# Performance work log

Measured on AMD Instinct MI355X. Metric: run time of the kernel, lower is better.

## Reference

```python
import jax, jax.numpy as jnp
import numpy as np

B, N, M, D = 2, 256, 8, 256      # batch, seq, modalities, dmodel
H, DH = 8, 64                     # heads, dim_head (hardcoded defaults)
INNER = H * DH                    # 512
MULT = 4                          # FFN mult
SCALE = DH ** -0.5
EPS = 1e-5


def layer_norm(x, g, b):
    mu = jnp.mean(x, axis=-1, keepdims=True)
    var = jnp.mean((x - mu) ** 2, axis=-1, keepdims=True)
    return (x - mu) * jax.lax.rsqrt(var + EPS) * g + b


def setup_inputs() -> dict:
    key = jax.random.key(0)
    ks = jax.random.split(key, 8)
    s = 0.02
    return {
        "x": jax.random.normal(ks[0], (B, D, M, N), jnp.float32),
        "Wq": jax.random.normal(ks[1], (D, INNER), jnp.float32) * s,
        "Wkv": jax.random.normal(ks[2], (D, 2 * INNER), jnp.float32) * s,
        "Wout": jax.random.normal(ks[3], (INNER * M, D * M), jnp.float32) * s,
        "bout": jnp.zeros((D * M,), jnp.float32),
        "g1": jnp.ones((D,), jnp.float32),
        "beta1": jnp.zeros((D,), jnp.float32),
        "Wff1": jax.random.normal(ks[4], (D, 2 * D * MULT), jnp.float32) * s,
        "bff1": jnp.zeros((2 * D * MULT,), jnp.float32),
        "Wff2": jax.random.normal(ks[5], (D * MULT, D), jnp.float32) * s,
        "bff2": jnp.zeros((D,), jnp.float32),
        "g2": jnp.ones((D,), jnp.float32),
        "beta2": jnp.zeros((D,), jnp.float32),
    }


def reference(x, Wq, Wkv, Wout, bout, g1, beta1, Wff1, bff1, Wff2, bff2, g2, beta2):
    x_shape = x.shape
    xt = jnp.transpose(x, (0, 3, 2, 1))          # [B,N,M,D]
    # --- Channel_Seq_Big_Attention (self-attention, context = x) ---
    q = (xt @ Wq).reshape(B, N, M, H, DH)
    kv = xt @ Wkv
    k, v = jnp.split(kv, 2, axis=-1)
    k = k.reshape(B, N, M, H, DH)
    v = v.reshape(B, N, M, H, DH)
    # sim: [(b h), i, j, m, z] kept as [B,H,i,j,m,z]
    sim = jnp.einsum('bimhd,bjzhd->bhijmz', q, k) * SCALE
    attn = jax.nn.softmax(sim, axis=2)           # softmax over j (dim=-3 of bijmz)
    out = jnp.einsum('bhijmz,bjmhd->bizhd', attn, v)  # [B,N,M,H,DH]
    out = out.reshape(B, N, M * H * DH)          # 'b n (m h d)'
    o = (out @ Wout + bout).reshape(B, N, M, D)
    # --- residual + post-norm ---
    xt = layer_norm(xt + o, g1, beta1)
    # --- GEGLU FFN ---
    hg = xt @ Wff1 + bff1
    a, gate = jnp.split(hg, 2, axis=-1)
    ff = (a * jax.nn.gelu(gate, approximate=False)) @ Wff2 + bff2
    xt = layer_norm(xt + ff, g2, beta2)
    return xt.reshape(x_shape)                   # torch .view(x_shape)
```

## Files before the change

kernel.cpp:

```cpp
#include <hip/hip_runtime.h>
#include <math.h>

#define KS_ 0.1803368801111244f

typedef __attribute__((ext_vector_type(8))) short bf16x8;
typedef __attribute__((ext_vector_type(4))) short bf16x4;
typedef __attribute__((ext_vector_type(4))) float f32x4;

__device__ inline short f2bf(float f) {
  unsigned u = __builtin_bit_cast(unsigned, f);
  u += 0x7fff + ((u >> 16) & 1);
  return (short)(u >> 16);
}

__global__ __launch_bounds__(256) void k_transpose(const float* __restrict__ x, float* __restrict__ xt,
                                                   short* __restrict__ xtbf) {
  __shared__ float tile[32][33];
  int bm = blockIdx.z; int b = bm >> 3; int m = bm & 7;
  int d0 = blockIdx.x * 32, n0 = blockIdx.y * 32;
#pragma unroll
  for (int r = 0; r < 32; r += 8) {
    int d = d0 + threadIdx.y + r, n = n0 + threadIdx.x;
    tile[threadIdx.y + r][threadIdx.x] = x[((size_t)(b * 256 + d) * 8 + m) * 256 + n];
  }
  __syncthreads();
#pragma unroll
  for (int r = 0; r < 32; r += 8) {
    int n = n0 + threadIdx.y + r, d = d0 + threadIdx.x;
    float v = tile[threadIdx.x][threadIdx.y + r];
    size_t idx = ((size_t)(b * 256 + n) * 8 + m) * 256 + d;
    xt[idx] = v;
    xtbf[idx] = f2bf(v);
  }
}

__global__ __launch_bounds__(256) void k_wt(const float* __restrict__ W, short* __restrict__ WT, int K, int N) {
  __shared__ float tile[32][33];
  int n0 = blockIdx.x * 32, k0 = blockIdx.y * 32;
  int tx = threadIdx.x & 31, ty = threadIdx.x >> 5;
#pragma unroll
  for (int r = 0; r < 32; r += 8)
    tile[ty + r][tx] = W[(size_t)(k0 + ty + r) * N + n0 + tx];
  __syncthreads();
#pragma unroll
  for (int r = 0; r < 32; r += 8)
    WT[(size_t)(n0 + ty + r) * K + k0 + tx] = f2bf(tile[tx][ty + r]);
}

__global__ __launch_bounds__(256) void k_gemm_bf(const short* __restrict__ A, const short* __restrict__ Bt,
                                                 const float* __restrict__ bias, float* __restrict__ C,
                                                 int M, int N, int K, int Ks) {
  __shared__ short As[64 * 40];
  __shared__ short Bs[64 * 40];
  int t = threadIdx.x;
  int row0 = blockIdx.y * 64, col0 = blockIdx.x * 64;
  int kp = blockIdx.z;
  int kbeg = kp * Ks, kend = kbeg + Ks;
  int w = t >> 6, lane = t & 63, quad = lane >> 4, l16 = lane & 15;
  int wr = w >> 1, wc = w & 1;
  int lrow = t >> 2, lch = (t & 3) * 8;
  const short* Ap = A + (size_t)(row0 + lrow) * K + lch;
  const short* Bp = Bt + (size_t)(col0 + lrow) * K + lch;
  f32x4 acc[2][2] = {{{0,0,0,0},{0,0,0,0}},{{0,0,0,0},{0,0,0,0}}};
  bf16x8 av = *(const bf16x8*)(Ap + kbeg);
  bf16x8 bv = *(const bf16x8*)(Bp + kbeg);
  for (int k0 = kbeg; k0 < kend; k0 += 32) {
    *(bf16x8*)&As[lrow * 40 + lch] = av;
    *(bf16x8*)&Bs[lrow * 40 + lch] = bv;
    __syncthreads();
    if (k0 + 32 < kend) {
      av = *(const bf16x8*)(Ap + k0 + 32);
      bv = *(const bf16x8*)(Bp + k0 + 32);
    }
    bf16x8 af[2], bf[2];
#pragma unroll
    for (int rf = 0; rf < 2; rf++) af[rf] = *(const bf16x8*)&As[(wr * 32 + rf * 16 + l16) * 40 + quad * 8];
#pragma unroll
    for (int cf = 0; cf < 2; cf++) bf[cf] = *(const bf16x8*)&Bs[(wc * 32 + cf * 16 + l16) * 40 + quad * 8];
#pragma unroll
    for (int rf = 0; rf < 2; rf++)
#pragma unroll
      for (int cf = 0; cf < 2; cf++)
        acc[rf][cf] = __builtin_amdgcn_mfma_f32_16x16x32_bf16(af[rf], bf[cf], acc[rf][cf], 0, 0, 0);
    __syncthreads();
  }
  float* Cp = C + (size_t)kp * M * N;
#pragma unroll
  for (int rf = 0; rf < 2; rf++)
#pragma unroll
    for (int cf = 0; cf < 2; cf++) {
      int col = col0 + wc * 32 + cf * 16 + l16;
      float vb = (bias && kp == 0) ? bias[col] : 0.0f;
#pragma unroll
      for (int r = 0; r < 4; r++) {
        int row = row0 + wr * 32 + rf * 16 + quad * 4 + r;
        Cp[(size_t)row * N + col] = acc[rf][cf][r] + vb;
      }
    }
}

__global__ __launch_bounds__(256) void k_ff1g(const short* __restrict__ A, const short* __restrict__ Bt,
                                              const float* __restrict__ bias, short* __restrict__ gg) {
  __shared__ short As[64 * 40];
  __shared__ short Ba[64 * 40];
  __shared__ short Bg[64 * 40];
  int t = threadIdx.x;
  int colA0 = blockIdx.x * 64, row0 = blockIdx.y * 64;
  int w = t >> 6, lane = t & 63, quad = lane >> 4, l16 = lane & 15;
  int wr = w >> 1, wc = w & 1;
  int lrow = t >> 2, lch = (t & 3) * 8;
  const short* Ap  = A + (size_t)(row0 + lrow) * 256 + lch;
  const short* Bpa = Bt + (size_t)(colA0 + lrow) * 256 + lch;
  const short* Bpg = Bt + (size_t)(1024 + colA0 + lrow) * 256 + lch;
  f32x4 za = {0, 0, 0, 0};
  f32x4 acc_a[2][2] = {{za, za}, {za, za}};
  f32x4 acc_g[2][2] = {{za, za}, {za, za}};
  bf16x8 av = *(const bf16x8*)(Ap);
  bf16x8 bva = *(const bf16x8*)(Bpa);
  bf16x8 bvg = *(const bf16x8*)(Bpg);
  for (int k0 = 0; k0 < 256; k0 += 32) {
    *(bf16x8*)&As[lrow * 40 + lch] = av;
    *(bf16x8*)&Ba[lrow * 40 + lch] = bva;
    *(bf16x8*)&Bg[lrow * 40 + lch] = bvg;
    __syncthreads();
    if (k0 + 32 < 256) {
      av  = *(const bf16x8*)(Ap + k0 + 32);
      bva = *(const bf16x8*)(Bpa + k0 + 32);
      bvg = *(const bf16x8*)(Bpg + k0 + 32);
    }
    bf16x8 af[2], ba[2], bg[2];
#pragma unroll
    for (int rf = 0; rf < 2; rf++) af[rf] = *(const bf16x8*)&As[(wr * 32 + rf * 16 + l16) * 40 + quad * 8];
#pragma unroll
    for (int cf = 0; cf < 2; cf++) {
      ba[cf] = *(const bf16x8*)&Ba[(wc * 32 + cf * 16 + l16) * 40 + quad * 8];
      bg[cf] = *(const bf16x8*)&Bg[(wc * 32 + cf * 16 + l16) * 40 + quad * 8];
    }
#pragma unroll
    for (int rf = 0; rf < 2; rf++)
#pragma unroll
      for (int cf = 0; cf < 2; cf++) {
        acc_a[rf][cf] = __builtin_amdgcn_mfma_f32_16x16x32_bf16(af[rf], ba[cf], acc_a[rf][cf], 0, 0, 0);
        acc_g[rf][cf] = __builtin_amdgcn_mfma_f32_16x16x32_bf16(af[rf], bg[cf], acc_g[rf][cf], 0, 0, 0);
      }
    __syncthreads();
  }
#pragma unroll
  for (int rf = 0; rf < 2; rf++)
#pragma unroll
    for (int cf = 0; cf < 2; cf++) {
      int col = colA0 + wc * 32 + cf * 16 + l16;
      float ba_ = bias[col], bg_ = bias[1024 + col];
#pragma unroll
      for (int r = 0; r < 4; r++) {
        int row = row0 + wr * 32 + rf * 16 + quad * 4 + r;
        float a = acc_a[rf][cf][r] + ba_;
        float g = acc_g[rf][cf][r] + bg_;
        float ge = 0.5f * g * (1.0f + erff(g * 0.70710678118654752f));
        gg[(size_t)row * 1024 + col] = f2bf(a * ge);
      }
    }
}

__global__ __launch_bounds__(256) void k_prep_qfrag(const float* __restrict__ qkv, short* __restrict__ qfrag) {
  int c = blockIdx.x * 256 + threadIdx.x;
  int lane = c & 63, ks = (c >> 6) & 1, rt = (c >> 7) & 127, bh = c >> 14;
  int b = bh >> 3, h = bh & 7;
  int m = rt >> 4, i = ((rt & 15) << 4) + (lane & 15);
  int d = ks * 32 + (lane >> 4) * 8;
  const float* src = qkv + (size_t)((b * 256 + i) * 8 + m) * 1536 + h * 64 + d;
  float4 f0 = *(const float4*)src, f1 = *(const float4*)(src + 4);
  bf16x8 o;
  o[0] = f2bf(f0.x); o[1] = f2bf(f0.y); o[2] = f2bf(f0.z); o[3] = f2bf(f0.w);
  o[4] = f2bf(f1.x); o[5] = f2bf(f1.y); o[6] = f2bf(f1.z); o[7] = f2bf(f1.w);
  *(bf16x8*)(qfrag + (size_t)c * 8) = o;
}

__global__ __launch_bounds__(256) void k_prep_kfrag(const float* __restrict__ qkv, short* __restrict__ kfrag) {
  int c = blockIdx.x * 256 + threadIdx.x;
  int lane = c & 63, ks = (c >> 6) & 1, rt = (c >> 7) & 127, bh = c >> 14;
  int b = bh >> 3, h = bh & 7;
  int z = rt >> 4, j = ((rt & 15) << 4) + (lane & 15);
  int d = ks * 32 + (lane >> 4) * 8;
  const float* src = qkv + (size_t)((b * 256 + j) * 8 + z) * 1536 + 512 + h * 64 + d;
  float4 f0 = *(const float4*)src, f1 = *(const float4*)(src + 4);
  bf16x8 o;
  o[0] = f2bf(f0.x); o[1] = f2bf(f0.y); o[2] = f2bf(f0.z); o[3] = f2bf(f0.w);
  o[4] = f2bf(f1.x); o[5] = f2bf(f1.y); o[6] = f2bf(f1.z); o[7] = f2bf(f1.w);
  *(bf16x8*)(kfrag + (size_t)c * 8) = o;
}

__global__ __launch_bounds__(256) void k_prep_vfrag(const float* __restrict__ qkv, short* __restrict__ vfrag) {
  __shared__ float Vs[256 * 66];
  int jc = blockIdx.x, bh = blockIdx.y;
  int b = bh >> 3, h = bh & 7;
  int t = threadIdx.x;
#pragma unroll
  for (int cc = 0; cc < 16; cc++) {
    int c = cc * 256 + t;
    int row = c >> 4, ch = c & 15;
    int m = row >> 5, jl = row & 31;
    float4 f = *(const float4*)(qkv + (size_t)((b * 256 + jc * 32 + jl) * 8 + m) * 1536 + 1024 + h * 64 + ch * 4);
    *(float4*)&Vs[row * 66 + ch * 4] = f;
  }
  __syncthreads();
  int m0 = t >> 6, lane = t & 63, quad = lane >> 4, l16 = lane & 15;
#pragma unroll
  for (int dt = 0; dt < 4; dt++)
#pragma unroll
    for (int jf = 0; jf < 2; jf++) {
      bf16x8 o;
#pragma unroll
      for (int e = 0; e < 8; e++) {
        int row = (2 * m0 + (e >> 2)) * 32 + jf * 16 + quad * 4 + (e & 3);
        o[e] = f2bf(Vs[row * 66 + dt * 16 + l16]);
      }
      size_t cid = ((((size_t)(bh * 8 + jc) * 4 + m0) * 4 + dt) * 2 + jf) * 64 + lane;
      *(bf16x8*)(vfrag + cid * 8) = o;
    }
}

__global__ __launch_bounds__(256) void k_attn_den5(const short* __restrict__ qfrag, const short* __restrict__ kfrag,
                                                   float* __restrict__ rdg) {
  int ct2 = blockIdx.x, mp = blockIdx.y, bh = blockIdx.z;
  int t = threadIdx.x;
  int w = t >> 6, lane = t & 63;
  int rt0 = ct2 * 8 + w * 2;
  bf16x8 bfr[2][2];
#pragma unroll
  for (int cf = 0; cf < 2; cf++)
#pragma unroll
    for (int ks = 0; ks < 2; ks++)
      bfr[cf][ks] = *(const bf16x8*)(kfrag + ((size_t)((bh * 128 + rt0 + cf) * 2 + ks)) * 512 + lane * 8);
  for (int mi = 0; mi < 2; mi++) {
    int m = mp * 2 + mi;
    float fa0 = 0.0f, fa1 = 0.0f;
#pragma unroll 4
    for (int it2 = 0; it2 < 16; it2++) {
      const short* ap = qfrag + ((size_t)((bh * 128 + m * 16 + it2) * 2)) * 512 + lane * 8;
      bf16x8 a0 = *(const bf16x8*)ap;
      bf16x8 a1 = *(const bf16x8*)(ap + 512);
      f32x4 c0 = {0, 0, 0, 0}, c1 = {0, 0, 0, 0};
      c0 = __builtin_amdgcn_mfma_f32_16x16x32_bf16(a0, bfr[0][0], c0, 0, 0, 0);
      c0 = __builtin_amdgcn_mfma_f32_16x16x32_bf16(a1, bfr[0][1], c0, 0, 0, 0);
      c1 = __builtin_amdgcn_mfma_f32_16x16x32_bf16(a0, bfr[1][0], c1, 0, 0, 0);
      c1 = __builtin_amdgcn_mfma_f32_16x16x32_bf16(a1, bfr[1][1], c1, 0, 0, 0);
#pragma unroll
      for (int r = 0; r < 4; r++) {
        fa0 += __builtin_amdgcn_exp2f(c0[r] * KS_);
        fa1 += __builtin_amdgcn_exp2f(c1[r] * KS_);
      }
    }
    fa0 += __shfl_xor(fa0, 16); fa0 += __shfl_xor(fa0, 32);
    fa1 += __shfl_xor(fa1, 16); fa1 += __shfl_xor(fa1, 32);
    if (lane < 16) {
      rdg[(size_t)(bh * 8 + m) * 2048 + rt0 * 16 + lane] = -__builtin_amdgcn_logf(fa0);
      rdg[(size_t)(bh * 8 + m) * 2048 + (rt0 + 1) * 16 + lane] = -__builtin_amdgcn_logf(fa1);
    }
  }
}

__global__ __launch_bounds__(256) void k_attn_out5(const short* __restrict__ qfrag, const short* __restrict__ kfrag,
                                                   const short* __restrict__ vfrag, const float* __restrict__ rdg,
                                                   short* __restrict__ ao) {
  __shared__ float red[4 * 64 * 17];
  int z = blockIdx.x, itp = blockIdx.y, bh = blockIdx.z;
  int b = bh >> 3, h = bh & 7;
  int t = threadIdx.x, w = t >> 6, lane = t & 63, quad = lane >> 4, l16 = lane & 15;
  const float* rb = rdg + (size_t)bh * 16384;
  f32x4 z4 = {0, 0, 0, 0};
  bf16x8 qf[2][2][2];
#pragma unroll
  for (int iti = 0; iti < 2; iti++)
#pragma unroll
    for (int mm = 0; mm < 2; mm++)
#pragma unroll
      for (int ks = 0; ks < 2; ks++)
        qf[iti][mm][ks] = *(const bf16x8*)(qfrag +
            ((size_t)((bh * 128 + (2 * w + mm) * 16 + itp * 2 + iti) * 2 + ks)) * 512 + lane * 8);
  f32x4 acc[2][4];
#pragma unroll
  for (int iti = 0; iti < 2; iti++)
#pragma unroll
    for (int dt = 0; dt < 4; dt++) acc[iti][dt] = z4;
  for (int jc = 0; jc < 8; jc++) {
    bf16x8 vf[4][2];
#pragma unroll
    for (int dt = 0; dt < 4; dt++)
#pragma unroll
      for (int jf = 0; jf < 2; jf++)
        vf[dt][jf] = *(const bf16x8*)(vfrag + ((((size_t)(bh * 8 + jc) * 4 + w) * 4 + dt) * 2 + jf) * 512 + lane * 8);
    bf16x8 kf[2][2];
#pragma unroll
    for (int jf = 0; jf < 2; jf++) {
      const short* kp = kfrag + ((size_t)((bh * 128 + z * 16 + jc * 2 + jf) * 2)) * 512 + lane * 8;
      kf[jf][0] = *(const bf16x8*)kp;
      kf[jf][1] = *(const bf16x8*)(kp + 512);
    }
    float n0[2][4], n1[2][4];
#pragma unroll
    for (int jf = 0; jf < 2; jf++) {
      float4 nv0 = *(const float4*)(rb + (size_t)(2 * w) * 2048 + z * 256 + jc * 32 + jf * 16 + quad * 4);
      float4 nv1 = *(const float4*)(rb + (size_t)(2 * w + 1) * 2048 + z * 256 + jc * 32 + jf * 16 + quad * 4);
      n0[jf][0] = nv0.x; n0[jf][1] = nv0.y; n0[jf][2] = nv0.z; n0[jf][3] = nv0.w;
      n1[jf][0] = nv1.x; n1[jf][1] = nv1.y; n1[jf][2] = nv1.z; n1[jf][3] = nv1.w;
    }
#pragma unroll
    for (int iti = 0; iti < 2; iti++) {
      f32x4 c[2][2] = {{z4, z4}, {z4, z4}};
#pragma unroll
      for (int jf = 0; jf < 2; jf++)
#pragma unroll
        for (int mm = 0; mm < 2; mm++) {
          c[jf][mm] = __builtin_amdgcn_mfma_f32_16x16x32_bf16(kf[jf][0], qf[iti][mm][0], c[jf][mm], 0, 0, 0);
          c[jf][mm] = __builtin_amdgcn_mfma_f32_16x16x32_bf16(kf[jf][1], qf[iti][mm][1], c[jf][mm], 0, 0, 0);
        }
      bf16x8 pf[2];
#pragma unroll
      for (int jf = 0; jf < 2; jf++) {
        unsigned u[8];
#pragma unroll
        for (int e = 0; e < 4; e++) {
          u[e]     = __builtin_bit_cast(unsigned, __builtin_amdgcn_exp2f(fmaf(c[jf][0][e], KS_, n0[jf][e]))) + 0x8000u;
          u[e + 4] = __builtin_bit_cast(unsigned, __builtin_amdgcn_exp2f(fmaf(c[jf][1][e], KS_, n1[jf][e]))) + 0x8000u;
        }
        uint4 pv;
        pv.x = __builtin_amdgcn_perm(u[1], u[0], 0x07060302u);
        pv.y = __builtin_amdgcn_perm(u[3], u[2], 0x07060302u);
        pv.z = __builtin_amdgcn_perm(u[5], u[4], 0x07060302u);
        pv.w = __builtin_amdgcn_perm(u[7], u[6], 0x07060302u);
        pf[jf] = __builtin_bit_cast(bf16x8, pv);
      }
#pragma unroll
      for (int dt = 0; dt < 4; dt++)
#pragma unroll
        for (int jf = 0; jf < 2; jf++)
          acc[iti][dt] = __builtin_amdgcn_mfma_f32_16x16x32_bf16(vf[dt][jf], pf[jf], acc[iti][dt], 0, 0, 0);
    }
  }
  for (int iti = 0; iti < 2; iti++) {
#pragma unroll
    for (int dt = 0; dt < 4; dt++)
#pragma unroll
      for (int r = 0; r < 4; r++)
        red[w * 1088 + (dt * 16 + quad * 4 + r) * 17 + l16] = acc[iti][dt][r];
    __syncthreads();
    {
      int i = t >> 4, dg = t & 15;
      float s[4] = {0, 0, 0, 0};
#pragma unroll
      for (int w2 = 0; w2 < 4; w2++)
#pragma unroll
        for (int r2 = 0; r2 < 4; r2++)
          s[r2] += red[w2 * 1088 + (dg * 4 + r2) * 17 + i];
      bf16x4 ov;
#pragma unroll
      for (int r2 = 0; r2 < 4; r2++) ov[r2] = f2bf(s[r2]);
      *(bf16x4*)(ao + (size_t)((b * 256 + itp * 32 + iti * 16 + i) * 8 + z) * 512 + h * 64 + dg * 4) = ov;
    }
    __syncthreads();
  }
}

__global__ __launch_bounds__(256) void k_ln(const float* __restrict__ X, const float* __restrict__ P, int np,
                                            const float* __restrict__ g, const float* __restrict__ be,
                                            float* __restrict__ Y, short* __restrict__ Ybf) {
  __shared__ float sm[8];
  int row = blockIdx.x, t = threadIdx.x;
  int lane = t & 63, w = t >> 6;
  size_t base = (size_t)row * 256;
  float v = X[base + t];
  for (int p = 0; p < np; p++) v += P[(size_t)p * 1048576 + base + t];
  float s = v;
  s += __shfl_xor(s, 1); s += __shfl_xor(s, 2); s += __shfl_xor(s, 4);
  s += __shfl_xor(s, 8); s += __shfl_xor(s, 16); s += __shfl_xor(s, 32);
  if (lane == 0) sm[w] = s;
  __syncthreads();
  float mu = (sm[0] + sm[1] + sm[2] + sm[3]) * (1.0f / 256.0f);
  float dv = v - mu;
  float s2 = dv * dv;
  s2 += __shfl_xor(s2, 1); s2 += __shfl_xor(s2, 2); s2 += __shfl_xor(s2, 4);
  s2 += __shfl_xor(s2, 8); s2 += __shfl_xor(s2, 16); s2 += __shfl_xor(s2, 32);
  if (lane == 0) sm[4 + w] = s2;
  __syncthreads();
  float var = (sm[4] + sm[5] + sm[6] + sm[7]) * (1.0f / 256.0f);
  float rs = rsqrtf(var + 1e-5f);
  float res = dv * rs * g[t] + be[t];
  Y[base + t] = res;
  if (Ybf) Ybf[base + t] = f2bf(res);
}

extern "C" void kernel_launch(void* const* d_in, const int* in_sizes, int n_in,
                              void* d_out, int out_size, void* d_ws, size_t ws_size,
                              hipStream_t stream) {
  const float* x    = (const float*)d_in[0];
  const float* Wq   = (const float*)d_in[1];
  const float* Wkv  = (const float*)d_in[2];
  const float* Wout = (const float*)d_in[3];
  const float* bout = (const float*)d_in[4];
  const float* g1   = (const float*)d_in[5];
  const float* be1  = (const float*)d_in[6];
  const float* Wff1 = (const float*)d_in[7];
  const float* bff1 = (const float*)d_in[8];
  const float* Wff2 = (const float*)d_in[9];
  const float* bff2 = (const float*)d_in[10];
  const float* g2   = (const float*)d_in[11];
  const float* be2  = (const float*)d_in[12];
  float* out = (float*)d_out;
  float* w = (float*)d_ws;

  float* xt   = w;
  float* qkv  = w + 1048576;
  float* part = w + 1048576;
  float* y    = w + 9437184;
  float* rdg  = w + 11534336;
  short* sb     = (short*)(w + 11796480);
  short* qfrag  = sb;
  short* kfrag  = sb + 2097152;
  short* vfrag  = sb + 4194304;
  short* xt_bf  = sb + 6291456;
  short* ao_bf  = sb + 7340032;
  short* y_bf   = sb + 9437184;
  short* gg_bf  = sb + 10485760;
  short* WqkvT  = sb + 14680064;
  short* WoutT  = sb + 15073280;
  short* Wff1T  = sb + 23461888;
  short* Wff2T  = sb + 23986176;

  k_transpose<<<dim3(8, 8, 16), dim3(32, 8), 0, stream>>>(x, xt, xt_bf);
  k_wt<<<dim3(16, 8), 256, 0, stream>>>(Wq, WqkvT, 256, 512);
  k_wt<<<dim3(32, 8), 256, 0, stream>>>(Wkv, WqkvT + 131072, 256, 1024);
  k_wt<<<dim3(64, 128), 256, 0, stream>>>(Wout, WoutT, 4096, 2048);
  k_wt<<<dim3(64, 8), 256, 0, stream>>>(Wff1, Wff1T, 256, 2048);
  k_wt<<<dim3(8, 32), 256, 0, stream>>>(Wff2, Wff2T, 1024, 256);
  k_gemm_bf<<<dim3(24, 64, 1), 256, 0, stream>>>(xt_bf, WqkvT, nullptr, qkv, 4096, 1536, 256, 256);
  k_prep_qfrag<<<1024, 256, 0, stream>>>(qkv, qfrag);
  k_prep_kfrag<<<1024, 256, 0, stream>>>(qkv, kfrag);
  k_prep_vfrag<<<dim3(8, 16), 256, 0, stream>>>(qkv, vfrag);
  k_attn_den5<<<dim3(16, 4, 16), 256, 0, stream>>>(qfrag, kfrag, rdg);
  k_attn_out5<<<dim3(8, 8, 16), 256, 0, stream>>>(qfrag, kfrag, vfrag, rdg, ao_bf);
  k_gemm_bf<<<dim3(32, 8, 4), 256, 0, stream>>>(ao_bf, WoutT, bout, part, 512, 2048, 4096, 1024);
  k_ln<<<4096, 256, 0, stream>>>(xt, part, 4, g1, be1, y, y_bf);
  k_ff1g<<<dim3(16, 64), 256, 0, stream>>>(y_bf, Wff1T, bff1, gg_bf);
  k_gemm_bf<<<dim3(4, 64, 4), 256, 0, stream>>>(gg_bf, Wff2T, bff2, part, 4096, 256, 1024, 256);
  k_ln<<<4096, 256, 0, stream>>>(y, part, 4, g2, be2, out, nullptr);
}
```

Measured before the change: 239.3 us.

## Merge prep kernels into single launches and prefetch next K/V chunk in attention

Six transpose/weight-conversion launches are folded into one block-indexed k_prep_all kernel, and the Q and K fragment prep kernels become one launch selected by block index. This cuts launch count and the idle gaps between small kernels. In the attention output kernel, V/K fragments and normalizer values for the next j-chunk are loaded before the current chunk's MFMAs run, so global load latency overlaps compute. The cost is higher register pressure in that kernel, which may lower occupancy.

```diff
diff --git a/kernel.cpp b/kernel.cpp
--- a/kernel.cpp
+++ b/kernel.cpp
@@ -13,31 +13,10 @@
   return (short)(u >> 16);
 }
 
-__global__ __launch_bounds__(256) void k_transpose(const float* __restrict__ x, float* __restrict__ xt,
-                                                   short* __restrict__ xtbf) {
-  __shared__ float tile[32][33];
-  int bm = blockIdx.z; int b = bm >> 3; int m = bm & 7;
-  int d0 = blockIdx.x * 32, n0 = blockIdx.y * 32;
-#pragma unroll
-  for (int r = 0; r < 32; r += 8) {
-    int d = d0 + threadIdx.y + r, n = n0 + threadIdx.x;
-    tile[threadIdx.y + r][threadIdx.x] = x[((size_t)(b * 256 + d) * 8 + m) * 256 + n];
-  }
-  __syncthreads();
-#pragma unroll
-  for (int r = 0; r < 32; r += 8) {
-    int n = n0 + threadIdx.y + r, d = d0 + threadIdx.x;
-    float v = tile[threadIdx.x][threadIdx.y + r];
-    size_t idx = ((size_t)(b * 256 + n) * 8 + m) * 256 + d;
-    xt[idx] = v;
-    xtbf[idx] = f2bf(v);
-  }
-}
-
-__global__ __launch_bounds__(256) void k_wt(const float* __restrict__ W, short* __restrict__ WT, int K, int N) {
-  __shared__ float tile[32][33];
-  int n0 = blockIdx.x * 32, k0 = blockIdx.y * 32;
-  int tx = threadIdx.x & 31, ty = threadIdx.x >> 5;
+__device__ inline void wt_tile(const float* __restrict__ W, short* __restrict__ WT,
+                               int K, int N, int bx, int by, int t, float (*tile)[33]) {
+  int n0 = bx * 32, k0 = by * 32;
+  int tx = t & 31, ty = t >> 5;
 #pragma unroll
   for (int r = 0; r < 32; r += 8)
     tile[ty + r][tx] = W[(size_t)(k0 + ty + r) * N + n0 + tx];
@@ -45,6 +24,52 @@
 #pragma unroll
   for (int r = 0; r < 32; r += 8)
     WT[(size_t)(n0 + ty + r) * K + k0 + tx] = f2bf(tile[tx][ty + r]);
+}
+
+__global__ __launch_bounds__(256) void k_prep_all(const float* __restrict__ x, float* __restrict__ xt,
+                                                  short* __restrict__ xtbf,
+                                                  const float* __restrict__ Wq, const float* __restrict__ Wkv,
+                                                  const float* __restrict__ Wout, const float* __restrict__ Wff1,
+                                                  const float* __restrict__ Wff2,
+                                                  short* __restrict__ WqkvT, short* __restrict__ WoutT,
+                                                  short* __restrict__ Wff1T, short* __restrict__ Wff2T) {
+  __shared__ float tile[32][33];
+  int bid = blockIdx.x, t = threadIdx.x;
+  if (bid < 8192) {
+    wt_tile(Wout, WoutT, 4096, 2048, bid & 63, bid >> 6, t, tile);
+  } else if (bid < 9216) {
+    int r = bid - 8192;
+    int bx = r & 7, by = (r >> 3) & 7, bm = r >> 6;
+    int b = bm >> 3, m = bm & 7;
+    int d0 = bx * 32, n0 = by * 32;
+    int tx = t & 31, ty = t >> 5;
+#pragma unroll
+    for (int rr = 0; rr < 32; rr += 8) {
+      int d = d0 + ty + rr, n = n0 + tx;
+      tile[ty + rr][tx] = x[((size_t)(b * 256 + d) * 8 + m) * 256 + n];
+    }
+    __syncthreads();
+#pragma unroll
+    for (int rr = 0; rr < 32; rr += 8) {
+      int n = n0 + ty + rr, d = d0 + tx;
+      float v = tile[tx][ty + rr];
+      size_t idx = ((size_t)(b * 256 + n) * 8 + m) * 256 + d;
+      xt[idx] = v;
+      xtbf[idx] = f2bf(v);
+    }
+  } else if (bid < 9344) {
+    int r = bid - 9216;
+    wt_tile(Wq, WqkvT, 256, 512, r & 15, r >> 4, t, tile);
+  } else if (bid < 9600) {
+    int r = bid - 9344;
+    wt_tile(Wkv, WqkvT + 131072, 256, 1024, r & 31, r >> 5, t, tile);
+  } else if (bid < 10112) {
+    int r = bid - 9600;
+    wt_tile(Wff1, Wff1T, 256, 2048, r & 63, r >> 6, t, tile);
+  } else {
+    int r = bid - 10112;
+    wt_tile(Wff2, Wff2T, 1024, 256, r & 7, r >> 3, t, tile);
+  }
 }
 
 __global__ __launch_bounds__(256) void k_gemm_bf(const short* __restrict__ A, const short* __restrict__ Bt,
@@ -162,32 +187,22 @@
     }
 }
 
-__global__ __launch_bounds__(256) void k_prep_qfrag(const float* __restrict__ qkv, short* __restrict__ qfrag) {
-  int c = blockIdx.x * 256 + threadIdx.x;
+__global__ __launch_bounds__(256) void k_prep_qk(const float* __restrict__ qkv, short* __restrict__ qfrag,
+                                                 short* __restrict__ kfrag) {
+  int bid = blockIdx.x;
+  int sel = bid >> 10;
+  int c = (bid & 1023) * 256 + threadIdx.x;
   int lane = c & 63, ks = (c >> 6) & 1, rt = (c >> 7) & 127, bh = c >> 14;
   int b = bh >> 3, h = bh & 7;
-  int m = rt >> 4, i = ((rt & 15) << 4) + (lane & 15);
+  int mz = rt >> 4, ij = ((rt & 15) << 4) + (lane & 15);
   int d = ks * 32 + (lane >> 4) * 8;
-  const float* src = qkv + (size_t)((b * 256 + i) * 8 + m) * 1536 + h * 64 + d;
+  const float* src = qkv + (size_t)((b * 256 + ij) * 8 + mz) * 1536 + sel * 512 + h * 64 + d;
   float4 f0 = *(const float4*)src, f1 = *(const float4*)(src + 4);
   bf16x8 o;
   o[0] = f2bf(f0.x); o[1] = f2bf(f0.y); o[2] = f2bf(f0.z); o[3] = f2bf(f0.w);
   o[4] = f2bf(f1.x); o[5] = f2bf(f1.y); o[6] = f2bf(f1.z); o[7] = f2bf(f1.w);
-  *(bf16x8*)(qfrag + (size_t)c * 8) = o;
-}
-
-__global__ __launch_bounds__(256) void k_prep_kfrag(const float* __restrict__ qkv, short* __restrict__ kfrag) {
-  int c = blockIdx.x * 256 + threadIdx.x;
-  int lane = c & 63, ks = (c >> 6) & 1, rt = (c >> 7) & 127, bh = c >> 14;
-  int b = bh >> 3, h = bh & 7;
-  int z = rt >> 4, j = ((rt & 15) << 4) + (lane & 15);
-  int d = ks * 32 + (lane >> 4) * 8;
-  const float* src = qkv + (size_t)((b * 256 + j) * 8 + z) * 1536 + 512 + h * 64 + d;
-  float4 f0 = *(const float4*)src, f1 = *(const float4*)(src + 4);
-  bf16x8 o;
-  o[0] = f2bf(f0.x); o[1] = f2bf(f0.y); o[2] = f2bf(f0.z); o[3] = f2bf(f0.w);
-  o[4] = f2bf(f1.x); o[5] = f2bf(f1.y); o[6] = f2bf(f1.z); o[7] = f2bf(f1.w);
-  *(bf16x8*)(kfrag + (size_t)c * 8) = o;
+  short* dst = sel ? kfrag : qfrag;
+  *(bf16x8*)(dst + (size_t)c * 8) = o;
 }
 
 __global__ __launch_bounds__(256) void k_prep_vfrag(const float* __restrict__ qkv, short* __restrict__ vfrag) {
@@ -260,7 +275,7 @@
   }
 }
 
-__global__ __launch_bounds__(256) void k_attn_out5(const short* __restrict__ qfrag, const short* __restrict__ kfrag,
+__global__ __launch_bounds__(256) void k_attn_out6(const short* __restrict__ qfrag, const short* __restrict__ kfrag,
                                                    const short* __restrict__ vfrag, const float* __restrict__ rdg,
                                                    short* __restrict__ ao) {
   __shared__ float red[4 * 64 * 17];
@@ -283,28 +298,42 @@
   for (int iti = 0; iti < 2; iti++)
 #pragma unroll
     for (int dt = 0; dt < 4; dt++) acc[iti][dt] = z4;
+  bf16x8 vf[4][2], kf[2][2];
+  float4 nv0[2], nv1[2];
+#pragma unroll
+  for (int dt = 0; dt < 4; dt++)
+#pragma unroll
+    for (int jf = 0; jf < 2; jf++)
+      vf[dt][jf] = *(const bf16x8*)(vfrag + ((((size_t)(bh * 8 + 0) * 4 + w) * 4 + dt) * 2 + jf) * 512 + lane * 8);
+#pragma unroll
+  for (int jf = 0; jf < 2; jf++) {
+    const short* kp = kfrag + ((size_t)((bh * 128 + z * 16 + 0 * 2 + jf) * 2)) * 512 + lane * 8;
+    kf[jf][0] = *(const bf16x8*)kp;
+    kf[jf][1] = *(const bf16x8*)(kp + 512);
+    nv0[jf] = *(const float4*)(rb + (size_t)(2 * w) * 2048 + z * 256 + 0 * 32 + jf * 16 + quad * 4);
+    nv1[jf] = *(const float4*)(rb + (size_t)(2 * w + 1) * 2048 + z * 256 + 0 * 32 + jf * 16 + quad * 4);
+  }
   for (int jc = 0; jc < 8; jc++) {
-    bf16x8 vf[4][2];
-#pragma unroll
-    for (int dt = 0; dt < 4; dt++)
-#pragma unroll
-      for (int jf = 0; jf < 2; jf++)
-        vf[dt][jf] = *(const bf16x8*)(vfrag + ((((size_t)(bh * 8 + jc) * 4 + w) * 4 + dt) * 2 + jf) * 512 + lane * 8);
-    bf16x8 kf[2][2];
-#pragma unroll
-    for (int jf = 0; jf < 2; jf++) {
-      const short* kp = kfrag + ((size_t)((bh * 128 + z * 16 + jc * 2 + jf) * 2)) * 512 + lane * 8;
-      kf[jf][0] = *(const bf16x8*)kp;
-      kf[jf][1] = *(const bf16x8*)(kp + 512);
-    }
-    float n0[2][4], n1[2][4];
-#pragma unroll
-    for (int jf = 0; jf < 2; jf++) {
-      float4 nv0 = *(const float4*)(rb + (size_t)(2 * w) * 2048 + z * 256 + jc * 32 + jf * 16 + quad * 4);
-      float4 nv1 = *(const float4*)(rb + (size_t)(2 * w + 1) * 2048 + z * 256 + jc * 32 + jf * 16 + quad * 4);
-      n0[jf][0] = nv0.x; n0[jf][1] = nv0.y; n0[jf][2] = nv0.z; n0[jf][3] = nv0.w;
-      n1[jf][0] = nv1.x; n1[jf][1] = nv1.y; n1[jf][2] = nv1.z; n1[jf][3] = nv1.w;
-    }
+    bf16x8 vfn[4][2], kfn[2][2];
+    float4 nv0n[2], nv1n[2];
+    if (jc < 7) {
+      int jn = jc + 1;
+#pragma unroll
+      for (int dt = 0; dt < 4; dt++)
+#pragma unroll
+        for (int jf = 0; jf < 2; jf++)
+          vfn[dt][jf] = *(const bf16x8*)(vfrag + ((((size_t)(bh * 8 + jn) * 4 + w) * 4 + dt) * 2 + jf) * 512 + lane * 8);
+#pragma unroll
+      for (int jf = 0; jf < 2; jf++) {
+        const short* kp = kfrag + ((size_t)((bh * 128 + z * 16 + jn * 2 + jf) * 2)) * 512 + lane * 8;
+        kfn[jf][0] = *(const bf16x8*)kp;
+        kfn[jf][1] = *(const bf16x8*)(kp + 512);
+        nv0n[jf] = *(const float4*)(rb + (size_t)(2 * w) * 2048 + z * 256 + jn * 32 + jf * 16 + quad * 4);
+        nv1n[jf] = *(const float4*)(rb + (size_t)(2 * w + 1) * 2048 + z * 256 + jn * 32 + jf * 16 + quad * 4);
+      }
+    }
+    float n0[2][4] = {{nv0[0].x, nv0[0].y, nv0[0].z, nv0[0].w}, {nv0[1].x, nv0[1].y, nv0[1].z, nv0[1].w}};
+    float n1[2][4] = {{nv1[0].x, nv1[0].y, nv1[0].z, nv1[0].w}, {nv1[1].x, nv1[1].y, nv1[1].z, nv1[1].w}};
 #pragma unroll
     for (int iti = 0; iti < 2; iti++) {
       f32x4 c[2][2] = {{z4, z4}, {z4, z4}};
@@ -336,6 +365,17 @@
 #pragma unroll
         for (int jf = 0; jf < 2; jf++)
           acc[iti][dt] = __builtin_amdgcn_mfma_f32_16x16x32_bf16(vf[dt][jf], pf[jf], acc[iti][dt], 0, 0, 0);
+    }
+    if (jc < 7) {
+#pragma unroll
+      for (int dt = 0; dt < 4; dt++)
+#pragma unroll
+        for (int jf = 0; jf < 2; jf++) vf[dt][jf] = vfn[dt][jf];
+#pragma unroll
+      for (int jf = 0; jf < 2; jf++) {
+        kf[jf][0] = kfn[jf][0]; kf[jf][1] = kfn[jf][1];
+        nv0[jf] = nv0n[jf]; nv1[jf] = nv1n[jf];
+      }
     }
   }
   for (int iti = 0; iti < 2; iti++) {
@@ -427,18 +467,13 @@
   short* Wff1T  = sb + 23461888;
   short* Wff2T  = sb + 23986176;
 
-  k_transpose<<<dim3(8, 8, 16), dim3(32, 8), 0, stream>>>(x, xt, xt_bf);
-  k_wt<<<dim3(16, 8), 256, 0, stream>>>(Wq, WqkvT, 256, 512);
-  k_wt<<<dim3(32, 8), 256, 0, stream>>>(Wkv, WqkvT + 131072, 256, 1024);
-  k_wt<<<dim3(64, 128), 256, 0, stream>>>(Wout, WoutT, 4096, 2048);
-  k_wt<<<dim3(64, 8), 256, 0, stream>>>(Wff1, Wff1T, 256, 2048);
-  k_wt<<<dim3(8, 32), 256, 0, stream>>>(Wff2, Wff2T, 1024, 256);
+  k_prep_all<<<10368, 256, 0, stream>>>(x, xt, xt_bf, Wq, Wkv, Wout, Wff1, Wff2,
+                                        WqkvT, WoutT, Wff1T, Wff2T);
   k_gemm_bf<<<dim3(24, 64, 1), 256, 0, stream>>>(xt_bf, WqkvT, nullptr, qkv, 4096, 1536, 256, 256);
-  k_prep_qfrag<<<1024, 256, 0, stream>>>(qkv, qfrag);
-  k_prep_kfrag<<<1024, 256, 0, stream>>>(qkv, kfrag);
+  k_prep_qk<<<2048, 256, 0, stream>>>(qkv, qfrag, kfrag);
   k_prep_vfrag<<<dim3(8, 16), 256, 0, stream>>>(qkv, vfrag);
   k_attn_den5<<<dim3(16, 4, 16), 256, 0, stream>>>(qfrag, kfrag, rdg);
-  k_attn_out5<<<dim3(8, 8, 16), 256, 0, stream>>>(qfrag, kfrag, vfrag, rdg, ao_bf);
+  k_attn_out6<<<dim3(8, 8, 16), 256, 0, stream>>>(qfrag, kfrag, vfrag, rdg, ao_bf);
   k_gemm_bf<<<dim3(32, 8, 4), 256, 0, stream>>>(ao_bf, WoutT, bout, part, 512, 2048, 4096, 1024);
   k_ln<<<4096, 256, 0, stream>>>(xt, part, 4, g1, be1, y, y_bf);
   k_ff1g<<<dim3(16, 64), 256, 0, stream>>>(y_bf, Wff1T, bff1, gg_bf);
```

Measured after the change: 230.9 us. -3.5%, faster.
